# Performance work log

Hardware: AMD Instinct MI355X
Metric: run time of the kernel (lower is better)

Reference implementation:

```python
import jax, jax.numpy as jnp
import numpy as np

B, N, C = 8, 1024, 768
H = 12
HD = C // H
RANK = 8
SCALE = HD ** -0.5


def setup_inputs() -> dict:
    key = jax.random.key(0)
    ks = jax.random.split(key, 12)
    s = C ** -0.5
    inp = {
        'x': jax.random.normal(ks[0], (B, N, C), jnp.float32),
        'w_qkv': jax.random.normal(ks[1], (3 * C, C), jnp.float32) * s,
        'b_qkv': jax.random.normal(ks[2], (3 * C,), jnp.float32) * 0.02,
        'w_proj': jax.random.normal(ks[3], (C, C), jnp.float32) * s,
        'b_proj': jax.random.normal(ks[4], (C,), jnp.float32) * 0.02,
        # LoRA A matrices (kaiming-uniform-ish); B matrices are zero at init,
        # but use small nonzero values so the adapter path is exercised.
        'q_a': jax.random.normal(ks[5], (RANK, C), jnp.float32) * s,
        'q_b': jax.random.normal(ks[6], (C, RANK), jnp.float32) * 0.01,
        'k_a': jax.random.normal(ks[7], (RANK, C), jnp.float32) * s,
        'k_b': jax.random.normal(ks[8], (C, RANK), jnp.float32) * 0.01,
        'v_a': jax.random.normal(ks[9], (RANK, C), jnp.float32) * s,
        'v_b': jax.random.normal(ks[10], (C, RANK), jnp.float32) * 0.01,
        'o_a': jax.random.normal(ks[11], (RANK, C), jnp.float32) * s,
        'o_b': jax.random.normal(jax.random.fold_in(key, 99), (C, RANK), jnp.float32) * 0.01,
    }
    return inp


def _lora(x, wa, wb):
    # x:[B,N,C], wa:[r,C], wb:[C,r] -> [B,N,C]
    return jnp.einsum('bnr,cr->bnc', jnp.einsum('bnc,rc->bnr', x, wa), wb)


def reference(x, w_qkv, b_qkv, w_proj, b_proj, q_a, q_b, k_a, k_b, v_a, v_b, o_a, o_b):
    # QKV projection + fused LoRA slice-adds
    qkv = jnp.einsum('bnc,dc->bnd', x, w_qkv) + b_qkv  # [B,N,3C]
    q = qkv[:, :, :C] + _lora(x, q_a, q_b)
    k = qkv[:, :, C:2 * C] + _lora(x, k_a, k_b)
    v = qkv[:, :, 2 * C:] + _lora(x, v_a, v_b)
    # [B,H,N,HD]
    q = q.reshape(B, N, H, HD).transpose(0, 2, 1, 3)
    k = k.reshape(B, N, H, HD).transpose(0, 2, 1, 3)
    v = v.reshape(B, N, H, HD).transpose(0, 2, 1, 3)
    attn = jnp.einsum('bhqd,bhkd->bhqk', q, k) * SCALE
    attn = jax.nn.softmax(attn, axis=-1)  # dropout is identity in eval
    o = jnp.einsum('bhqk,bhkd->bhqd', attn, v)
    o = o.transpose(0, 2, 1, 3).reshape(B, N, C)
    out = jnp.einsum('bnc,dc->bnd', o, w_proj) + b_proj + _lora(o, o_a, o_b)
    return out
```

## Files before the change

kernel.cpp:

```cpp
#include <hip/hip_runtime.h>

typedef __attribute__((ext_vector_type(8))) short short8;
typedef __attribute__((ext_vector_type(4))) float f32x4;
typedef __attribute__((ext_vector_type(4))) unsigned short u16x4;
typedef __attribute__((ext_vector_type(2))) unsigned int u32x2;

#define MFMA16(a,b,c) __builtin_amdgcn_mfma_f32_16x16x32_bf16((a),(b),(c),0,0,0)

#define QSCALE 0.1803368801f

__device__ __forceinline__ unsigned short f2bf(float f) {
  unsigned int x = __float_as_uint(f);
  x += 0x7fffu + ((x >> 16) & 1u);
  return (unsigned short)(x >> 16);
}
__device__ __forceinline__ unsigned int pack2bf(float a, float b) {
  unsigned int ua = __float_as_uint(a) + 0x8000u;
  unsigned int ub = __float_as_uint(b) + 0x8000u;
  return __builtin_amdgcn_perm(ub, ua, 0x07060302);
}
__device__ __forceinline__ void gload16(const unsigned short* g, unsigned short* l) {
  __builtin_amdgcn_global_load_lds(
      (const __attribute__((address_space(1))) unsigned int*)g,
      (__attribute__((address_space(3))) unsigned int*)l, 16, 0, 0);
}

__global__ __launch_bounds__(256) void prep(
    const float* __restrict__ x,
    const float* __restrict__ w_qkv,
    const float* __restrict__ w_proj,
    const float* __restrict__ q_a, const float* __restrict__ q_b,
    const float* __restrict__ k_a, const float* __restrict__ k_b,
    const float* __restrict__ v_a, const float* __restrict__ v_b,
    const float* __restrict__ o_a, const float* __restrict__ o_b,
    unsigned short* __restrict__ xb,
    unsigned short* __restrict__ wqkv_eff,
    unsigned short* __restrict__ wproj_eff)
{
  int bid = blockIdx.x;
  if (bid < 6144) {
    int i4 = (bid * 256 + threadIdx.x) * 4;
    f32x4 v = *(const f32x4*)&x[i4];
    u16x4 o;
    o.x = f2bf(v.x); o.y = f2bf(v.y); o.z = f2bf(v.z); o.w = f2bf(v.w);
    *(u16x4*)&xb[i4] = o;
    return;
  }
  const int QKV = 2304 * 768;
  int idx = (bid - 6144) * 256 + threadIdx.x;
  if (idx < QKV) {
    int n = idx / 768, c = idx - n * 768;
    int sec = n / 768;
    int nr = n - sec * 768;
    const float* a; const float* b;
    if (sec == 0)      { a = q_a; b = q_b; }
    else if (sec == 1) { a = k_a; b = k_b; }
    else               { a = v_a; b = v_b; }
    float acc = w_qkv[idx];
    #pragma unroll
    for (int r = 0; r < 8; r++)
      acc += b[nr * 8 + r] * a[r * 768 + c];
    wqkv_eff[idx] = f2bf(acc);
  } else {
    int i2 = idx - QKV;
    int n = i2 / 768, c = i2 - n * 768;
    float acc = w_proj[i2];
    #pragma unroll
    for (int r = 0; r < 8; r++)
      acc += o_b[n * 8 + r] * o_a[r * 768 + c];
    wproj_eff[i2] = f2bf(acc);
  }
}

__global__ __launch_bounds__(256) void gemm_bt(
    const unsigned short* __restrict__ A,
    const unsigned short* __restrict__ W,
    const float* __restrict__ bias,
    unsigned short* __restrict__ out0,
    unsigned short* __restrict__ out1,
    unsigned short* __restrict__ out2,
    float* __restrict__ outf,
    int K, int Ncols, int mode)
{
  __shared__ alignas(16) unsigned short As[128 * 64];
  __shared__ alignas(16) unsigned short Ws[128 * 64];
  const int tid  = threadIdx.x;
  const int wave = tid >> 6;
  const int lane = tid & 63;
  const int quad = lane >> 4;
  const int l16  = lane & 15;
  const int wr   = wave >> 1, wc = wave & 1;
  const int m0 = blockIdx.x * 128;
  const int n0 = blockIdx.y * 128;

  const int lrow   = lane >> 3;
  const int lchunk = (lane & 7) ^ lrow;
  const unsigned short* gA[4];
  const unsigned short* gW[4];
  unsigned short* lA[4];
  unsigned short* lW[4];
  #pragma unroll
  for (int t = 0; t < 4; t++) {
    int rr = wave * 32 + t * 8;
    gA[t] = A + (size_t)(m0 + rr + lrow) * K + lchunk * 8;
    gW[t] = W + (size_t)(n0 + rr + lrow) * K + lchunk * 8;
    lA[t] = &As[(rr + lrow) * 64 + (lane & 7) * 8];
    lW[t] = &Ws[(rr + lrow) * 64 + (lane & 7) * 8];
  }

  f32x4 acc[4][4] = {};
  const int swz = (l16 & 7);

  for (int k0 = 0; k0 < K; k0 += 64) {
    #pragma unroll
    for (int t = 0; t < 4; t++) {
      gload16(gA[t] + k0, lA[t]);
      gload16(gW[t] + k0, lW[t]);
    }
    __syncthreads();
    #pragma unroll
    for (int ks = 0; ks < 2; ks++) {
      const int cs = ks * 4 + quad;
      short8 a[4], b[4];
      #pragma unroll
      for (int t = 0; t < 4; t++) {
        a[t] = *(const short8*)&As[(wr * 64 + t * 16 + l16) * 64 + ((cs ^ swz) << 3)];
        b[t] = *(const short8*)&Ws[(wc * 64 + t * 16 + l16) * 64 + ((cs ^ swz) << 3)];
      }
      #pragma unroll
      for (int i = 0; i < 4; i++)
        #pragma unroll
        for (int j = 0; j < 4; j++)
          acc[i][j] = MFMA16(a[i], b[j], acc[i][j]);
    }
    __syncthreads();
  }

  float bv[4];
  #pragma unroll
  for (int j = 0; j < 4; j++) bv[j] = bias[n0 + wc * 64 + j * 16 + l16];

  if (mode == 0) {
    const int sec = n0 / 768;
    const int h   = ((n0 % 768) >> 6) + wc;
    unsigned short* dst = (sec == 0) ? out0 : ((sec == 1) ? out1 : out2);
    const float scl = (sec == 0) ? QSCALE : 1.0f;
    #pragma unroll
    for (int i = 0; i < 4; i++) {
      #pragma unroll
      for (int r = 0; r < 4; r++) {
        int m  = m0 + wr * 64 + i * 16 + quad * 4 + r;
        int bb = m >> 10, np = m & 1023;
        int bh = bb * 12 + h;
        int npp = (np & ~63) | ((np & 15) * 4 + ((np >> 4) & 3));
        #pragma unroll
        for (int j = 0; j < 4; j++) {
          int d = j * 16 + l16;
          float v = (acc[i][j][r] + bv[j]) * scl;
          if (sec < 2) dst[((size_t)bh << 16) + ((size_t)np << 6) + d] = f2bf(v);
          else         dst[((size_t)bh << 16) + ((size_t)d << 10) + npp] = f2bf(v);
        }
      }
    }
  } else {
    #pragma unroll
    for (int i = 0; i < 4; i++) {
      #pragma unroll
      for (int r = 0; r < 4; r++) {
        int m = m0 + wr * 64 + i * 16 + quad * 4 + r;
        #pragma unroll
        for (int j = 0; j < 4; j++)
          outf[(size_t)m * Ncols + n0 + wc * 64 + j * 16 + l16] = acc[i][j][r] + bv[j];
      }
    }
  }
}

__global__ __launch_bounds__(256) void attn(
    const unsigned short* __restrict__ q,
    const unsigned short* __restrict__ k,
    const unsigned short* __restrict__ vt,
    unsigned short* __restrict__ o)
{
  __shared__ alignas(16) unsigned short Qs[128][72];
  __shared__ alignas(16) unsigned short Ks[64][72];
  __shared__ alignas(16) unsigned short Vs[64][72];
  const int tid  = threadIdx.x;
  const int wave = tid >> 6;
  const int lane = tid & 63;
  const int quad = lane >> 4;
  const int l16  = lane & 15;
  const int bh = blockIdx.x;
  const int q0 = blockIdx.y * 128;
  const unsigned short* qb = q  + ((size_t)bh << 16);
  const unsigned short* kb = k  + ((size_t)bh << 16);
  const unsigned short* vb = vt + ((size_t)bh << 16);

  #pragma unroll
  for (int i = 0; i < 4; i++) {
    int flat = tid + i * 256;
    int r = flat >> 3, ck = (flat & 7) << 3;
    *(f32x4*)&Qs[r][ck] = *(const f32x4*)&qb[((size_t)(q0 + r) << 6) + ck];
  }
  __syncthreads();
  short8 aq[2][2];
  #pragma unroll
  for (int rg = 0; rg < 2; rg++)
    #pragma unroll
    for (int ks = 0; ks < 2; ks++)
      aq[rg][ks] = *(const short8*)&Qs[wave * 32 + rg * 16 + l16][ks * 32 + quad * 8];
  __syncthreads();
  unsigned short (*Ps)[72] = (unsigned short (*)[72])(&Qs[wave * 32][0]);

  f32x4 Oacc[2][4] = {};
  float lsum[2][4] = {};

  int sr[2], sc[2];
  #pragma unroll
  for (int i = 0; i < 2; i++) { int f = tid + i * 256; sr[i] = f >> 3; sc[i] = (f & 7) << 3; }

  f32x4 kreg[2], vreg[2];
  #pragma unroll
  for (int i = 0; i < 2; i++) {
    kreg[i] = *(const f32x4*)&kb[((size_t)sr[i] << 6) + sc[i]];
    vreg[i] = *(const f32x4*)&vb[((size_t)sr[i] << 10) + sc[i]];
  }

  for (int kt = 0; kt < 16; kt++) {
    __syncthreads();
    #pragma unroll
    for (int i = 0; i < 2; i++) {
      *(f32x4*)&Ks[sr[i]][sc[i]] = kreg[i];
      *(f32x4*)&Vs[sr[i]][sc[i]] = vreg[i];
    }
    __syncthreads();
    if (kt < 15) {
      #pragma unroll
      for (int i = 0; i < 2; i++) {
        kreg[i] = *(const f32x4*)&kb[((size_t)((kt + 1) * 64 + sr[i]) << 6) + sc[i]];
        vreg[i] = *(const f32x4*)&vb[((size_t)sr[i] << 10) + (kt + 1) * 64 + sc[i]];
      }
    }

    f32x4 s[2][4] = {};
    #pragma unroll
    for (int ks = 0; ks < 2; ks++) {
      const int kk = ks * 32 + quad * 8;
      short8 b0 = *(const short8*)&Ks[l16][kk];
      short8 b1 = *(const short8*)&Ks[16 + l16][kk];
      short8 b2 = *(const short8*)&Ks[32 + l16][kk];
      short8 b3 = *(const short8*)&Ks[48 + l16][kk];
      s[0][0] = MFMA16(aq[0][ks], b0, s[0][0]);
      s[0][1] = MFMA16(aq[0][ks], b1, s[0][1]);
      s[0][2] = MFMA16(aq[0][ks], b2, s[0][2]);
      s[0][3] = MFMA16(aq[0][ks], b3, s[0][3]);
      s[1][0] = MFMA16(aq[1][ks], b0, s[1][0]);
      s[1][1] = MFMA16(aq[1][ks], b1, s[1][1]);
      s[1][2] = MFMA16(aq[1][ks], b2, s[1][2]);
      s[1][3] = MFMA16(aq[1][ks], b3, s[1][3]);
    }

    #pragma unroll
    for (int rg = 0; rg < 2; rg++) {
      #pragma unroll
      for (int r = 0; r < 4; r++) {
        float p0 = exp2f(s[rg][0][r]);
        float p1 = exp2f(s[rg][1][r]);
        float p2 = exp2f(s[rg][2][r]);
        float p3 = exp2f(s[rg][3][r]);
        lsum[rg][r] += (p0 + p1) + (p2 + p3);
        u32x2 pk;
        pk.x = pack2bf(p0, p1);
        pk.y = pack2bf(p2, p3);
        *(u32x2*)&Ps[rg * 16 + quad * 4 + r][4 * l16] = pk;
      }
    }

    #pragma unroll
    for (int ks = 0; ks < 2; ks++) {
      const int kk = ks * 32 + quad * 8;
      short8 a0 = *(const short8*)&Ps[l16][kk];
      short8 a1 = *(const short8*)&Ps[16 + l16][kk];
      short8 v0 = *(const short8*)&Vs[l16][kk];
      short8 v1 = *(const short8*)&Vs[16 + l16][kk];
      short8 v2 = *(const short8*)&Vs[32 + l16][kk];
      short8 v3 = *(const short8*)&Vs[48 + l16][kk];
      Oacc[0][0] = MFMA16(a0, v0, Oacc[0][0]);
      Oacc[0][1] = MFMA16(a0, v1, Oacc[0][1]);
      Oacc[0][2] = MFMA16(a0, v2, Oacc[0][2]);
      Oacc[0][3] = MFMA16(a0, v3, Oacc[0][3]);
      Oacc[1][0] = MFMA16(a1, v0, Oacc[1][0]);
      Oacc[1][1] = MFMA16(a1, v1, Oacc[1][1]);
      Oacc[1][2] = MFMA16(a1, v2, Oacc[1][2]);
      Oacc[1][3] = MFMA16(a1, v3, Oacc[1][3]);
    }
  }

  const int b = bh / 12, h = bh - (bh / 12) * 12;
  #pragma unroll
  for (int rg = 0; rg < 2; rg++) {
    #pragma unroll
    for (int r = 0; r < 4; r++) {
      float t = lsum[rg][r];
      t += __shfl_xor(t, 1, 64);
      t += __shfl_xor(t, 2, 64);
      t += __shfl_xor(t, 4, 64);
      t += __shfl_xor(t, 8, 64);
      float inv = 1.0f / t;
      int np = q0 + wave * 32 + rg * 16 + quad * 4 + r;
      size_t base = ((size_t)(b * 1024 + np)) * 768 + h * 64;
      #pragma unroll
      for (int j = 0; j < 4; j++)
        o[base + j * 16 + l16] = f2bf(Oacc[rg][j][r] * inv);
    }
  }
}

extern "C" void kernel_launch(void* const* d_in, const int* in_sizes, int n_in,
                              void* d_out, int out_size, void* d_ws, size_t ws_size,
                              hipStream_t stream) {
  const float* x      = (const float*)d_in[0];
  const float* w_qkv  = (const float*)d_in[1];
  const float* b_qkv  = (const float*)d_in[2];
  const float* w_proj = (const float*)d_in[3];
  const float* b_proj = (const float*)d_in[4];
  const float* q_a    = (const float*)d_in[5];
  const float* q_b    = (const float*)d_in[6];
  const float* k_a    = (const float*)d_in[7];
  const float* k_b    = (const float*)d_in[8];
  const float* v_a    = (const float*)d_in[9];
  const float* v_b    = (const float*)d_in[10];
  const float* o_a    = (const float*)d_in[11];
  const float* o_b    = (const float*)d_in[12];

  char* ws = (char*)d_ws;
  unsigned short* wqkv_eff  = (unsigned short*)(ws + 0);
  unsigned short* wproj_eff = (unsigned short*)(ws + 3538944);
  unsigned short* xb        = (unsigned short*)(ws + 4718592);
  unsigned short* qd        = (unsigned short*)(ws + 17301504);
  unsigned short* kd        = (unsigned short*)(ws + 29884416);
  unsigned short* vtd       = (unsigned short*)(ws + 42467328);
  unsigned short* od        = xb;

  prep<<<dim3(6144 + 9216), dim3(256), 0, stream>>>(
      x, w_qkv, w_proj, q_a, q_b, k_a, k_b, v_a, v_b, o_a, o_b,
      xb, wqkv_eff, wproj_eff);

  gemm_bt<<<dim3(64, 18), dim3(256), 0, stream>>>(
      xb, wqkv_eff, b_qkv, qd, kd, vtd, nullptr, 768, 2304, 0);

  attn<<<dim3(96, 8), dim3(256), 0, stream>>>(qd, kd, vtd, od);

  gemm_bt<<<dim3(64, 6), dim3(256), 0, stream>>>(
      od, wproj_eff, b_proj, nullptr, nullptr, nullptr, (float*)d_out, 768, 768, 1);
}
```

Measured before the change: 224.0 us.

## Double-buffer W tiles in LDS and load A fragments directly into registers

Restructures the GEMM main loop so the W tile goes into a double-buffered LDS region while A fragments are read straight from global memory into registers, prefetching the next k-step while MFMAs run on the current one. This cuts one barrier per iteration and removes the A LDS round trip, and launch bounds now ask for three blocks per SM. The costs are duplicated A global reads across the two column waves, higher register pressure from 16 short8 A fragments, and the assumption that K/64 is even.

```diff
diff --git a/kernel.cpp b/kernel.cpp
--- a/kernel.cpp
+++ b/kernel.cpp
@@ -72,7 +72,37 @@
   }
 }
 
-__global__ __launch_bounds__(256) void gemm_bt(
+#define GEMM_STEP(kk, p, CUR, NXT)                                            \
+  {                                                                           \
+    __syncthreads();                                                          \
+    const int kn_ = ((kk) + 1) << 6;                                          \
+    if (kn_ < K) {                                                            \
+      _Pragma("unroll")                                                       \
+      for (int t = 0; t < 4; t++)                                             \
+        gload16(gW[t] + kn_, ws_ + (1 - (p)) * (128 * 64) + lw_off[t]);       \
+      _Pragma("unroll")                                                       \
+      for (int t = 0; t < 4; t++) {                                           \
+        NXT[2 * t]     = *(const short8*)&gA[(size_t)t * 16 * K + kn_];       \
+        NXT[2 * t + 1] = *(const short8*)&gA[(size_t)t * 16 * K + kn_ + 32];  \
+      }                                                                       \
+    }                                                                         \
+    _Pragma("unroll")                                                         \
+    for (int ks = 0; ks < 2; ks++) {                                          \
+      const int cs = ks * 4 + quad;                                           \
+      short8 b_[4];                                                           \
+      _Pragma("unroll")                                                       \
+      for (int t = 0; t < 4; t++)                                             \
+        b_[t] = *(const short8*)&ws_[(p) * (128 * 64) +                       \
+                 (wc * 64 + t * 16 + l16) * 64 + ((cs ^ swz) << 3)];          \
+      _Pragma("unroll")                                                       \
+      for (int i = 0; i < 4; i++)                                             \
+        _Pragma("unroll")                                                     \
+        for (int j = 0; j < 4; j++)                                           \
+          acc[i][j] = MFMA16(CUR[2 * i + ks], b_[j], acc[i][j]);              \
+    }                                                                         \
+  }
+
+__global__ __launch_bounds__(256, 3) void gemm_bt(
     const unsigned short* __restrict__ A,
     const unsigned short* __restrict__ W,
     const float* __restrict__ bias,
@@ -82,8 +112,8 @@
     float* __restrict__ outf,
     int K, int Ncols, int mode)
 {
-  __shared__ alignas(16) unsigned short As[128 * 64];
-  __shared__ alignas(16) unsigned short Ws[128 * 64];
+  __shared__ alignas(16) unsigned short Ws[2 * 128 * 64];
+  unsigned short* ws_ = &Ws[0];
   const int tid  = threadIdx.x;
   const int wave = tid >> 6;
   const int lane = tid & 63;
@@ -92,48 +122,35 @@
   const int wr   = wave >> 1, wc = wave & 1;
   const int m0 = blockIdx.x * 128;
   const int n0 = blockIdx.y * 128;
+  const int swz = l16 & 7;
 
   const int lrow   = lane >> 3;
   const int lchunk = (lane & 7) ^ lrow;
-  const unsigned short* gA[4];
   const unsigned short* gW[4];
-  unsigned short* lA[4];
-  unsigned short* lW[4];
+  int lw_off[4];
   #pragma unroll
   for (int t = 0; t < 4; t++) {
     int rr = wave * 32 + t * 8;
-    gA[t] = A + (size_t)(m0 + rr + lrow) * K + lchunk * 8;
-    gW[t] = W + (size_t)(n0 + rr + lrow) * K + lchunk * 8;
-    lA[t] = &As[(rr + lrow) * 64 + (lane & 7) * 8];
-    lW[t] = &Ws[(rr + lrow) * 64 + (lane & 7) * 8];
-  }
+    gW[t]     = W + (size_t)(n0 + rr + lrow) * K + lchunk * 8;
+    lw_off[t] = (rr + lrow) * 64 + (lane & 7) * 8;
+  }
+  const unsigned short* gA = A + (size_t)(m0 + wr * 64 + l16) * K + quad * 8;
 
   f32x4 acc[4][4] = {};
-  const int swz = (l16 & 7);
-
-  for (int k0 = 0; k0 < K; k0 += 64) {
-    #pragma unroll
-    for (int t = 0; t < 4; t++) {
-      gload16(gA[t] + k0, lA[t]);
-      gload16(gW[t] + k0, lW[t]);
-    }
-    __syncthreads();
-    #pragma unroll
-    for (int ks = 0; ks < 2; ks++) {
-      const int cs = ks * 4 + quad;
-      short8 a[4], b[4];
-      #pragma unroll
-      for (int t = 0; t < 4; t++) {
-        a[t] = *(const short8*)&As[(wr * 64 + t * 16 + l16) * 64 + ((cs ^ swz) << 3)];
-        b[t] = *(const short8*)&Ws[(wc * 64 + t * 16 + l16) * 64 + ((cs ^ swz) << 3)];
-      }
-      #pragma unroll
-      for (int i = 0; i < 4; i++)
-        #pragma unroll
-        for (int j = 0; j < 4; j++)
-          acc[i][j] = MFMA16(a[i], b[j], acc[i][j]);
-    }
-    __syncthreads();
+  short8 aA[8], aB[8];
+
+  #pragma unroll
+  for (int t = 0; t < 4; t++) gload16(gW[t], ws_ + lw_off[t]);
+  #pragma unroll
+  for (int t = 0; t < 4; t++) {
+    aA[2 * t]     = *(const short8*)&gA[(size_t)t * 16 * K];
+    aA[2 * t + 1] = *(const short8*)&gA[(size_t)t * 16 * K + 32];
+  }
+
+  const int nit = K >> 6;
+  for (int k = 0; k < nit; k += 2) {
+    GEMM_STEP(k,     0, aA, aB);
+    GEMM_STEP(k + 1, 1, aB, aA);
   }
 
   float bv[4];
```

Result: slower. 303.3 us (+35.4%).
